# Optimization experiments

Hardware: AMD Instinct MI355X
Metric: run time of the kernel (lower is better)

Reference implementation:

```python
import jax, jax.numpy as jnp
import numpy as np

def setup_inputs() -> dict:
    key = jax.random.key(0)
    ks = jax.random.split(key, 6)
    ch, cr = 256, 32  # cr = ch // 8
    B, H, W = 4, 64, 64
    sc = 1.0 / np.sqrt(ch)
    return {
        "inputs": jax.random.normal(ks[0], (B, H, W, ch), jnp.float32),
        "Wf": jax.random.normal(ks[1], (ch, cr), jnp.float32) * sc,
        "bf": jnp.zeros((cr,), jnp.float32),
        "Wg": jax.random.normal(ks[2], (ch, cr), jnp.float32) * sc,
        "bg": jnp.zeros((cr,), jnp.float32),
        "Wh": jax.random.normal(ks[3], (ch, cr), jnp.float32) * sc,
        "bh": jnp.zeros((cr,), jnp.float32),
        "Wv": jax.random.normal(ks[4], (cr, ch), jnp.float32) * (1.0 / np.sqrt(cr)),
        "bv": jnp.zeros((ch,), jnp.float32),
        "gamma": jnp.zeros((1,), jnp.float32),
    }

def reference(inputs, Wf, bf, Wg, bg, Wh, bh, Wv, bv, gamma):
    B, H, W, C = inputs.shape
    x = inputs.reshape(B, H * W, C)  # [B, N, C]
    f = x @ Wf + bf  # [B, N, cr] (keys)
    g = x @ Wg + bg  # [B, N, cr] (queries)
    h = x @ Wh + bh  # [B, N, cr] (values)
    s = jnp.einsum('bnk,bmk->bnm', g, f)  # [B, N, N]
    beta = jax.nn.softmax(s, axis=-1)
    v = jnp.einsum('bnm,bmk->bnk', beta, h)  # [B, N, cr]
    o = v @ Wv + bv  # [B, N, C]
    out = gamma * o + x
    return out.reshape(B, H, W, C)
```

## Files before the change

kernel.cpp:

```cpp
#include <hip/hip_runtime.h>

#define B_SZ  4
#define N_TOK 4096
#define CH    256
#define CR    32
#define SEG   512
#define KT    64
#define NITER (SEG / KT)
#define LOG2E 1.44269504f

typedef __attribute__((ext_vector_type(8))) short bf16x8;
typedef __attribute__((ext_vector_type(4))) float f32x4;

__device__ inline ushort f2bf(float x) {
    uint u = __float_as_uint(x);
    u += 0x7fff + ((u >> 16) & 1);
    return (ushort)(u >> 16);
}
__device__ inline uint pk2bf(float a, float b) {
    return __builtin_amdgcn_perm(__float_as_uint(b), __float_as_uint(a), 0x07060302);
}
__device__ inline float fast_exp2(float x) {
#if __has_builtin(__builtin_amdgcn_exp2f)
    return __builtin_amdgcn_exp2f(x);
#else
    return exp2f(x);
#endif
}

__global__ __launch_bounds__(256) void proj_kernel(
    const float* __restrict__ x,
    const float* __restrict__ Wf, const float* __restrict__ Wg, const float* __restrict__ Wh,
    const float* __restrict__ bf_, const float* __restrict__ bg, const float* __restrict__ bh,
    ushort* __restrict__ fo, ushort* __restrict__ go, ushort* __restrict__ hto)
{
    __shared__ ushort wst[3][32][264];
    int t = threadIdx.x;

    {
        float4 r4[8];
        const float* rf = (const float*)&r4[0];
        #pragma unroll
        for (int q4 = 0; q4 < 8; ++q4) r4[q4] = *(const float4*)(Wf + (size_t)t * CR + q4 * 4);
        #pragma unroll
        for (int j = 0; j < 32; ++j) wst[0][j][t] = f2bf(rf[j]);
        #pragma unroll
        for (int q4 = 0; q4 < 8; ++q4) r4[q4] = *(const float4*)(Wg + (size_t)t * CR + q4 * 4);
        #pragma unroll
        for (int j = 0; j < 32; ++j) wst[1][j][t] = f2bf(rf[j]);
        #pragma unroll
        for (int q4 = 0; q4 < 8; ++q4) r4[q4] = *(const float4*)(Wh + (size_t)t * CR + q4 * 4);
        #pragma unroll
        for (int j = 0; j < 32; ++j) wst[2][j][t] = f2bf(rf[j]);
    }
    __syncthreads();

    int wv = t >> 6, L = t & 63, nl = L & 15, Q = L >> 4;
    int row_t = blockIdx.x * 64 + wv * 16;
    int b = row_t >> 12, tok0 = row_t & 4095;

    const float* xrow = x + (size_t)(row_t + nl) * CH;
    f32x4 A[6];
    #pragma unroll
    for (int i = 0; i < 6; ++i) A[i] = (f32x4){0.f, 0.f, 0.f, 0.f};

    #pragma unroll
    for (int kk = 0; kk < 8; ++kk) {
        int off = kk * 32 + Q * 8;
        float4 lo = *(const float4*)(xrow + off);
        float4 hi = *(const float4*)(xrow + off + 4);
        bf16x8 xa;
        xa[0] = (short)f2bf(lo.x); xa[1] = (short)f2bf(lo.y);
        xa[2] = (short)f2bf(lo.z); xa[3] = (short)f2bf(lo.w);
        xa[4] = (short)f2bf(hi.x); xa[5] = (short)f2bf(hi.y);
        xa[6] = (short)f2bf(hi.z); xa[7] = (short)f2bf(hi.w);

        bf16x8 wf0 = *(const bf16x8*)&wst[0][nl][off];
        bf16x8 wf1 = *(const bf16x8*)&wst[0][16 + nl][off];
        bf16x8 wg0 = *(const bf16x8*)&wst[1][nl][off];
        bf16x8 wg1 = *(const bf16x8*)&wst[1][16 + nl][off];
        bf16x8 wh0 = *(const bf16x8*)&wst[2][nl][off];
        bf16x8 wh1 = *(const bf16x8*)&wst[2][16 + nl][off];

        A[0] = __builtin_amdgcn_mfma_f32_16x16x32_bf16(xa, wf0, A[0], 0, 0, 0);
        A[1] = __builtin_amdgcn_mfma_f32_16x16x32_bf16(xa, wf1, A[1], 0, 0, 0);
        A[2] = __builtin_amdgcn_mfma_f32_16x16x32_bf16(xa, wg0, A[2], 0, 0, 0);
        A[3] = __builtin_amdgcn_mfma_f32_16x16x32_bf16(xa, wg1, A[3], 0, 0, 0);
        A[4] = __builtin_amdgcn_mfma_f32_16x16x32_bf16(wh0, xa, A[4], 0, 0, 0);
        A[5] = __builtin_amdgcn_mfma_f32_16x16x32_bf16(wh1, xa, A[5], 0, 0, 0);
    }

    float bF0 = bf_[nl], bF1 = bf_[16 + nl];
    float bG0 = bg[nl] * LOG2E, bG1 = bg[16 + nl] * LOG2E;
    #pragma unroll
    for (int r = 0; r < 4; ++r) {
        size_t ro = (size_t)(row_t + Q * 4 + r) * CR;
        fo[ro + nl]      = f2bf(A[0][r] + bF0);
        fo[ro + 16 + nl] = f2bf(A[1][r] + bF1);
        go[ro + nl]      = f2bf(fmaf(A[2][r], LOG2E, bG0));
        go[ro + 16 + nl] = f2bf(fmaf(A[3][r], LOG2E, bG1));
    }
    ushort* hb = hto + (size_t)b * CR * N_TOK + tok0 + nl;
    #pragma unroll
    for (int r = 0; r < 4; ++r) {
        int ch = Q * 4 + r;
        hb[(size_t)ch * N_TOK]        = f2bf(A[4][r] + bh[ch]);
        hb[(size_t)(16 + ch) * N_TOK] = f2bf(A[5][r] + bh[16 + ch]);
    }
}

__global__ __launch_bounds__(512, 4) void attn_kernel(
    const ushort* __restrict__ f, const ushort* __restrict__ g,
    const ushort* __restrict__ ht, const float* __restrict__ Wv,
    const float* __restrict__ bv, const float* __restrict__ gamma,
    const float* __restrict__ x, float* __restrict__ out)
{
    __shared__ unsigned long long smem_raw[38912 / 8];
    ushort (*pls)[32][76]  = (ushort (*)[32][76])smem_raw;
    float  (*obuf)[32][33] = (float (*)[32][33])smem_raw;
    float  (*lbuf)[32]     = (float (*)[32])((char*)smem_raw + 33792);
    ushort (*oc)[48]       = (ushort (*)[48])((char*)smem_raw + 34816);

    int t  = threadIdx.x;
    int wv = t >> 6;
    int L  = t & 63;
    int nl = L & 15;
    int Q  = L >> 4;
    int bid = blockIdx.x;
    int swz = (bid & 7) * 64 + (bid >> 3);
    int b  = swz >> 7;
    int q0 = (swz & 127) * 32;

    const ushort* fb  = f  + (size_t)b * N_TOK * CR;
    const ushort* htb = ht + (size_t)b * CR * N_TOK;

    bf16x8 gB0 = *(const bf16x8*)(g + ((size_t)b * N_TOK + q0 + nl) * CR + Q * 8);
    bf16x8 gB1 = *(const bf16x8*)(g + ((size_t)b * N_TOK + q0 + 16 + nl) * CR + Q * 8);

    f32x4 acc00 = {0,0,0,0}, acc01 = {0,0,0,0};
    f32x4 acc10 = {0,0,0,0}, acc11 = {0,0,0,0};
    const f32x4 zf = {0,0,0,0};
    float lsum0 = 0.f, lsum1 = 0.f;

    int key0 = wv * SEG;
    bf16x8 Ac0 = *(const bf16x8*)(fb + (size_t)(key0 +  0 + nl) * CR + Q * 8);
    bf16x8 Ac1 = *(const bf16x8*)(fb + (size_t)(key0 + 16 + nl) * CR + Q * 8);
    bf16x8 Ac2 = *(const bf16x8*)(fb + (size_t)(key0 + 32 + nl) * CR + Q * 8);
    bf16x8 Ac3 = *(const bf16x8*)(fb + (size_t)(key0 + 48 + nl) * CR + Q * 8);

    #pragma unroll 2
    for (int it = 0; it < NITER; ++it) {
        int kc = wv * SEG + it * KT;
        const ushort* hk = htb + (size_t)nl * N_TOK + kc;
        bf16x8 b00 = *(const bf16x8*)(hk + Q * 8);
        bf16x8 b01 = *(const bf16x8*)(hk + (size_t)16 * N_TOK + Q * 8);
        bf16x8 b10 = *(const bf16x8*)(hk + 32 + Q * 8);
        bf16x8 b11 = *(const bf16x8*)(hk + (size_t)16 * N_TOK + 32 + Q * 8);
        int kn = wv * SEG + ((it + 1 < NITER) ? it + 1 : 0) * KT;
        const ushort* fn = fb + (size_t)kn * CR;
        bf16x8 An0 = *(const bf16x8*)(fn + (size_t)( 0 + nl) * CR + Q * 8);
        bf16x8 An1 = *(const bf16x8*)(fn + (size_t)(16 + nl) * CR + Q * 8);
        bf16x8 An2 = *(const bf16x8*)(fn + (size_t)(32 + nl) * CR + Q * 8);
        bf16x8 An3 = *(const bf16x8*)(fn + (size_t)(48 + nl) * CR + Q * 8);

        f32x4 s00 = __builtin_amdgcn_mfma_f32_16x16x32_bf16(Ac0, gB0, zf, 0, 0, 0);
        f32x4 s01 = __builtin_amdgcn_mfma_f32_16x16x32_bf16(Ac1, gB0, zf, 0, 0, 0);
        f32x4 s02 = __builtin_amdgcn_mfma_f32_16x16x32_bf16(Ac2, gB0, zf, 0, 0, 0);
        f32x4 s03 = __builtin_amdgcn_mfma_f32_16x16x32_bf16(Ac3, gB0, zf, 0, 0, 0);
        f32x4 s10 = __builtin_amdgcn_mfma_f32_16x16x32_bf16(Ac0, gB1, zf, 0, 0, 0);
        f32x4 s11 = __builtin_amdgcn_mfma_f32_16x16x32_bf16(Ac1, gB1, zf, 0, 0, 0);
        f32x4 s12 = __builtin_amdgcn_mfma_f32_16x16x32_bf16(Ac2, gB1, zf, 0, 0, 0);
        f32x4 s13 = __builtin_amdgcn_mfma_f32_16x16x32_bf16(Ac3, gB1, zf, 0, 0, 0);

        #pragma unroll
        for (int qh = 0; qh < 2; ++qh) {
            f32x4 v0 = qh ? s10 : s00, v1 = qh ? s11 : s01;
            f32x4 v2 = qh ? s12 : s02, v3 = qh ? s13 : s03;
            int row = qh * 16 + nl;
            float p0 = fast_exp2(v0[0]), p1 = fast_exp2(v0[1]);
            float p2 = fast_exp2(v0[2]), p3 = fast_exp2(v0[3]);
            float s4 = ((p0+p1)+(p2+p3));
            uint2 w; w.x = pk2bf(p0,p1); w.y = pk2bf(p2,p3);
            *(uint2*)&pls[wv][row][ 0 + Q * 4] = w;
            p0 = fast_exp2(v1[0]); p1 = fast_exp2(v1[1]);
            p2 = fast_exp2(v1[2]); p3 = fast_exp2(v1[3]);
            s4 += ((p0+p1)+(p2+p3));
            w.x = pk2bf(p0,p1); w.y = pk2bf(p2,p3);
            *(uint2*)&pls[wv][row][16 + Q * 4] = w;
            p0 = fast_exp2(v2[0]); p1 = fast_exp2(v2[1]);
            p2 = fast_exp2(v2[2]); p3 = fast_exp2(v2[3]);
            s4 += ((p0+p1)+(p2+p3));
            w.x = pk2bf(p0,p1); w.y = pk2bf(p2,p3);
            *(uint2*)&pls[wv][row][32 + Q * 4] = w;
            p0 = fast_exp2(v3[0]); p1 = fast_exp2(v3[1]);
            p2 = fast_exp2(v3[2]); p3 = fast_exp2(v3[3]);
            s4 += ((p0+p1)+(p2+p3));
            w.x = pk2bf(p0,p1); w.y = pk2bf(p2,p3);
            *(uint2*)&pls[wv][row][48 + Q * 4] = w;
            if (qh) lsum1 += s4; else lsum0 += s4;
        }

        bf16x8 aP00 = *(const bf16x8*)&pls[wv][     nl][ 0 + Q * 8];
        bf16x8 aP01 = *(const bf16x8*)&pls[wv][     nl][32 + Q * 8];
        bf16x8 aP10 = *(const bf16x8*)&pls[wv][16 + nl][ 0 + Q * 8];
        bf16x8 aP11 = *(const bf16x8*)&pls[wv][16 + nl][32 + Q * 8];

        acc00 = __builtin_amdgcn_mfma_f32_16x16x32_bf16(aP00, b00, acc00, 0, 0, 0);
        acc01 = __builtin_amdgcn_mfma_f32_16x16x32_bf16(aP00, b01, acc01, 0, 0, 0);
        acc10 = __builtin_amdgcn_mfma_f32_16x16x32_bf16(aP10, b00, acc10, 0, 0, 0);
        acc11 = __builtin_amdgcn_mfma_f32_16x16x32_bf16(aP10, b01, acc11, 0, 0, 0);
        acc00 = __builtin_amdgcn_mfma_f32_16x16x32_bf16(aP01, b10, acc00, 0, 0, 0);
        acc01 = __builtin_amdgcn_mfma_f32_16x16x32_bf16(aP01, b11, acc01, 0, 0, 0);
        acc10 = __builtin_amdgcn_mfma_f32_16x16x32_bf16(aP11, b10, acc10, 0, 0, 0);
        acc11 = __builtin_amdgcn_mfma_f32_16x16x32_bf16(aP11, b11, acc11, 0, 0, 0);

        Ac0 = An0; Ac1 = An1; Ac2 = An2; Ac3 = An3;
    }

    lsum0 += __shfl_xor(lsum0, 16); lsum0 += __shfl_xor(lsum0, 32);
    lsum1 += __shfl_xor(lsum1, 16); lsum1 += __shfl_xor(lsum1, 32);

    __syncthreads();
    #pragma unroll
    for (int r = 0; r < 4; ++r) {
        obuf[wv][     Q * 4 + r][nl]      = acc00[r];
        obuf[wv][     Q * 4 + r][16 + nl] = acc01[r];
        obuf[wv][16 + Q * 4 + r][nl]      = acc10[r];
        obuf[wv][16 + Q * 4 + r][16 + nl] = acc11[r];
    }
    if (L < 16) { lbuf[wv][nl] = lsum0; lbuf[wv][16 + nl] = lsum1; }
    __syncthreads();

    {
        int ch = t & 31, qb = t >> 5;
        #pragma unroll
        for (int qq = qb; qq < 32; qq += 16) {
            float s = 0.f, Lq = 0.f;
            #pragma unroll
            for (int w = 0; w < 8; ++w) { s += obuf[w][qq][ch]; Lq += lbuf[w][qq]; }
            oc[qq][ch] = f2bf(s / Lq);
        }
    }
    __syncthreads();

    bf16x8 aO0 = *(const bf16x8*)&oc[     nl][Q * 8];
    bf16x8 aO1 = *(const bf16x8*)&oc[16 + nl][Q * 8];
    float gm = gamma[0];
    const float* xb = x   + ((size_t)b * N_TOK + q0) * CH;
    float*       ob = out + ((size_t)b * N_TOK + q0) * CH;
    #pragma unroll
    for (int i = 0; i < 2; ++i) {
        int nb = wv * 2 + i;
        int c = nb * 16 + nl;
        const float* wvp = Wv + c;
        bf16x8 bW;
        #pragma unroll
        for (int j = 0; j < 8; ++j) bW[j] = (short)f2bf(wvp[(size_t)(Q * 8 + j) * CH]);
        f32x4 d0 = __builtin_amdgcn_mfma_f32_16x16x32_bf16(aO0, bW, zf, 0, 0, 0);
        f32x4 d1 = __builtin_amdgcn_mfma_f32_16x16x32_bf16(aO1, bW, zf, 0, 0, 0);
        float bvc = bv[c];
        #pragma unroll
        for (int r = 0; r < 4; ++r) {
            int qa = Q * 4 + r;
            ob[qa * CH + c]        = fmaf(gm, d0[r] + bvc, xb[qa * CH + c]);
            ob[(16 + qa) * CH + c] = fmaf(gm, d1[r] + bvc, xb[(16 + qa) * CH + c]);
        }
    }
}

extern "C" void kernel_launch(void* const* d_in, const int* in_sizes, int n_in,
                              void* d_out, int out_size, void* d_ws, size_t ws_size,
                              hipStream_t stream) {
    const float* x     = (const float*)d_in[0];
    const float* Wf    = (const float*)d_in[1];
    const float* bf_   = (const float*)d_in[2];
    const float* Wg    = (const float*)d_in[3];
    const float* bg    = (const float*)d_in[4];
    const float* Wh    = (const float*)d_in[5];
    const float* bh    = (const float*)d_in[6];
    const float* Wv    = (const float*)d_in[7];
    const float* bv    = (const float*)d_in[8];
    const float* gamma = (const float*)d_in[9];
    float* out = (float*)d_out;

    const size_t T = (size_t)B_SZ * N_TOK * CR;
    ushort* fo  = (ushort*)d_ws;
    ushort* go  = fo + T;
    ushort* hto = go + T;

    proj_kernel<<<B_SZ * N_TOK / 64, 256, 0, stream>>>(x, Wf, Wg, Wh, bf_, bg, bh, fo, go, hto);
    attn_kernel<<<B_SZ * (N_TOK / 32), 512, 0, stream>>>(fo, go, hto, Wv, bv, gamma, x, out);
}
```

Before: 120.8 us.

## Use 64-query blocks of 16 waves with halved key segments per wave

Each block now handles 64 queries with 1024 threads (16 waves), each wave covering a 256-key segment in 32-key steps against all 64 queries. Every loaded K/V tile is reused across four query groups rather than two, which halves global key/value traffic per query. The cross-wave reduction now runs in two phases: the upper 8 waves write partial accumulators and the lower 8 waves add theirs into the same buffer. In exchange, shared memory rises to about 80KB per block and blocks are larger, which may lower occupancy and increase synchronisation cost.

```diff
diff --git a/kernel.cpp b/kernel.cpp
--- a/kernel.cpp
+++ b/kernel.cpp
@@ -4,8 +4,8 @@
 #define N_TOK 4096
 #define CH    256
 #define CR    32
-#define SEG   512
-#define KT    64
+#define SEG   256
+#define KT    32
 #define NITER (SEG / KT)
 #define LOG2E 1.44269504f
 
@@ -109,17 +109,17 @@
     }
 }
 
-__global__ __launch_bounds__(512, 4) void attn_kernel(
+__global__ __launch_bounds__(1024, 4) void attn_kernel(
     const ushort* __restrict__ f, const ushort* __restrict__ g,
     const ushort* __restrict__ ht, const float* __restrict__ Wv,
     const float* __restrict__ bv, const float* __restrict__ gamma,
     const float* __restrict__ x, float* __restrict__ out)
 {
-    __shared__ unsigned long long smem_raw[38912 / 8];
-    ushort (*pls)[32][76]  = (ushort (*)[32][76])smem_raw;
-    float  (*obuf)[32][33] = (float (*)[32][33])smem_raw;
-    float  (*lbuf)[32]     = (float (*)[32])((char*)smem_raw + 33792);
-    ushort (*oc)[48]       = (ushort (*)[48])((char*)smem_raw + 34816);
+    __shared__ unsigned long long smem_raw[81920 / 8];
+    ushort (*pls)[64][40]  = (ushort (*)[64][40])smem_raw;
+    float  (*obuf)[64][33] = (float (*)[64][33])smem_raw;
+    float  (*lbuf)[64]     = (float (*)[64])((char*)smem_raw + 67584);
+    ushort (*oc)[48]       = (ushort (*)[48])((char*)smem_raw + 71680);
 
     int t  = threadIdx.x;
     int wv = t >> 6;
@@ -127,143 +127,137 @@
     int nl = L & 15;
     int Q  = L >> 4;
     int bid = blockIdx.x;
-    int swz = (bid & 7) * 64 + (bid >> 3);
-    int b  = swz >> 7;
-    int q0 = (swz & 127) * 32;
+    int swz = (bid & 7) * 32 + (bid >> 3);
+    int b  = swz >> 6;
+    int q0 = (swz & 63) * 64;
 
     const ushort* fb  = f  + (size_t)b * N_TOK * CR;
     const ushort* htb = ht + (size_t)b * CR * N_TOK;
 
-    bf16x8 gB0 = *(const bf16x8*)(g + ((size_t)b * N_TOK + q0 + nl) * CR + Q * 8);
-    bf16x8 gB1 = *(const bf16x8*)(g + ((size_t)b * N_TOK + q0 + 16 + nl) * CR + Q * 8);
-
-    f32x4 acc00 = {0,0,0,0}, acc01 = {0,0,0,0};
-    f32x4 acc10 = {0,0,0,0}, acc11 = {0,0,0,0};
+    bf16x8 gB[4];
+    #pragma unroll
+    for (int qh = 0; qh < 4; ++qh)
+        gB[qh] = *(const bf16x8*)(g + ((size_t)b * N_TOK + q0 + qh * 16 + nl) * CR + Q * 8);
+
+    f32x4 acc[4][2];
+    #pragma unroll
+    for (int i = 0; i < 4; ++i) { acc[i][0] = (f32x4){0,0,0,0}; acc[i][1] = (f32x4){0,0,0,0}; }
     const f32x4 zf = {0,0,0,0};
-    float lsum0 = 0.f, lsum1 = 0.f;
+    float ls0 = 0.f, ls1 = 0.f, ls2 = 0.f, ls3 = 0.f;
 
     int key0 = wv * SEG;
-    bf16x8 Ac0 = *(const bf16x8*)(fb + (size_t)(key0 +  0 + nl) * CR + Q * 8);
+    bf16x8 Ac0 = *(const bf16x8*)(fb + (size_t)(key0 +      nl) * CR + Q * 8);
     bf16x8 Ac1 = *(const bf16x8*)(fb + (size_t)(key0 + 16 + nl) * CR + Q * 8);
-    bf16x8 Ac2 = *(const bf16x8*)(fb + (size_t)(key0 + 32 + nl) * CR + Q * 8);
-    bf16x8 Ac3 = *(const bf16x8*)(fb + (size_t)(key0 + 48 + nl) * CR + Q * 8);
 
     #pragma unroll 2
     for (int it = 0; it < NITER; ++it) {
-        int kc = wv * SEG + it * KT;
+        int kc = key0 + it * KT;
         const ushort* hk = htb + (size_t)nl * N_TOK + kc;
-        bf16x8 b00 = *(const bf16x8*)(hk + Q * 8);
-        bf16x8 b01 = *(const bf16x8*)(hk + (size_t)16 * N_TOK + Q * 8);
-        bf16x8 b10 = *(const bf16x8*)(hk + 32 + Q * 8);
-        bf16x8 b11 = *(const bf16x8*)(hk + (size_t)16 * N_TOK + 32 + Q * 8);
-        int kn = wv * SEG + ((it + 1 < NITER) ? it + 1 : 0) * KT;
-        const ushort* fn = fb + (size_t)kn * CR;
-        bf16x8 An0 = *(const bf16x8*)(fn + (size_t)( 0 + nl) * CR + Q * 8);
-        bf16x8 An1 = *(const bf16x8*)(fn + (size_t)(16 + nl) * CR + Q * 8);
-        bf16x8 An2 = *(const bf16x8*)(fn + (size_t)(32 + nl) * CR + Q * 8);
-        bf16x8 An3 = *(const bf16x8*)(fn + (size_t)(48 + nl) * CR + Q * 8);
-
-        f32x4 s00 = __builtin_amdgcn_mfma_f32_16x16x32_bf16(Ac0, gB0, zf, 0, 0, 0);
-        f32x4 s01 = __builtin_amdgcn_mfma_f32_16x16x32_bf16(Ac1, gB0, zf, 0, 0, 0);
-        f32x4 s02 = __builtin_amdgcn_mfma_f32_16x16x32_bf16(Ac2, gB0, zf, 0, 0, 0);
-        f32x4 s03 = __builtin_amdgcn_mfma_f32_16x16x32_bf16(Ac3, gB0, zf, 0, 0, 0);
-        f32x4 s10 = __builtin_amdgcn_mfma_f32_16x16x32_bf16(Ac0, gB1, zf, 0, 0, 0);
-        f32x4 s11 = __builtin_amdgcn_mfma_f32_16x16x32_bf16(Ac1, gB1, zf, 0, 0, 0);
-        f32x4 s12 = __builtin_amdgcn_mfma_f32_16x16x32_bf16(Ac2, gB1, zf, 0, 0, 0);
-        f32x4 s13 = __builtin_amdgcn_mfma_f32_16x16x32_bf16(Ac3, gB1, zf, 0, 0, 0);
-
-        #pragma unroll
-        for (int qh = 0; qh < 2; ++qh) {
-            f32x4 v0 = qh ? s10 : s00, v1 = qh ? s11 : s01;
-            f32x4 v2 = qh ? s12 : s02, v3 = qh ? s13 : s03;
+        bf16x8 bh0 = *(const bf16x8*)(hk + Q * 8);
+        bf16x8 bh1 = *(const bf16x8*)(hk + (size_t)16 * N_TOK + Q * 8);
+        int kn = key0 + ((it + 1 < NITER) ? it + 1 : 0) * KT;
+        bf16x8 An0 = *(const bf16x8*)(fb + (size_t)(kn +      nl) * CR + Q * 8);
+        bf16x8 An1 = *(const bf16x8*)(fb + (size_t)(kn + 16 + nl) * CR + Q * 8);
+
+        #pragma unroll
+        for (int qh = 0; qh < 4; ++qh) {
+            f32x4 s0 = __builtin_amdgcn_mfma_f32_16x16x32_bf16(Ac0, gB[qh], zf, 0, 0, 0);
+            f32x4 s1 = __builtin_amdgcn_mfma_f32_16x16x32_bf16(Ac1, gB[qh], zf, 0, 0, 0);
             int row = qh * 16 + nl;
-            float p0 = fast_exp2(v0[0]), p1 = fast_exp2(v0[1]);
-            float p2 = fast_exp2(v0[2]), p3 = fast_exp2(v0[3]);
-            float s4 = ((p0+p1)+(p2+p3));
-            uint2 w; w.x = pk2bf(p0,p1); w.y = pk2bf(p2,p3);
+            float p0 = fast_exp2(s0[0]), p1 = fast_exp2(s0[1]);
+            float p2 = fast_exp2(s0[2]), p3 = fast_exp2(s0[3]);
+            float s4 = ((p0 + p1) + (p2 + p3));
+            uint2 w; w.x = pk2bf(p0, p1); w.y = pk2bf(p2, p3);
             *(uint2*)&pls[wv][row][ 0 + Q * 4] = w;
-            p0 = fast_exp2(v1[0]); p1 = fast_exp2(v1[1]);
-            p2 = fast_exp2(v1[2]); p3 = fast_exp2(v1[3]);
-            s4 += ((p0+p1)+(p2+p3));
-            w.x = pk2bf(p0,p1); w.y = pk2bf(p2,p3);
+            p0 = fast_exp2(s1[0]); p1 = fast_exp2(s1[1]);
+            p2 = fast_exp2(s1[2]); p3 = fast_exp2(s1[3]);
+            s4 += ((p0 + p1) + (p2 + p3));
+            w.x = pk2bf(p0, p1); w.y = pk2bf(p2, p3);
             *(uint2*)&pls[wv][row][16 + Q * 4] = w;
-            p0 = fast_exp2(v2[0]); p1 = fast_exp2(v2[1]);
-            p2 = fast_exp2(v2[2]); p3 = fast_exp2(v2[3]);
-            s4 += ((p0+p1)+(p2+p3));
-            w.x = pk2bf(p0,p1); w.y = pk2bf(p2,p3);
-            *(uint2*)&pls[wv][row][32 + Q * 4] = w;
-            p0 = fast_exp2(v3[0]); p1 = fast_exp2(v3[1]);
-            p2 = fast_exp2(v3[2]); p3 = fast_exp2(v3[3]);
-            s4 += ((p0+p1)+(p2+p3));
-            w.x = pk2bf(p0,p1); w.y = pk2bf(p2,p3);
-            *(uint2*)&pls[wv][row][48 + Q * 4] = w;
-            if (qh) lsum1 += s4; else lsum0 += s4;
+            if (qh == 0) ls0 += s4; else if (qh == 1) ls1 += s4;
+            else if (qh == 2) ls2 += s4; else ls3 += s4;
         }
 
-        bf16x8 aP00 = *(const bf16x8*)&pls[wv][     nl][ 0 + Q * 8];
-        bf16x8 aP01 = *(const bf16x8*)&pls[wv][     nl][32 + Q * 8];
-        bf16x8 aP10 = *(const bf16x8*)&pls[wv][16 + nl][ 0 + Q * 8];
-        bf16x8 aP11 = *(const bf16x8*)&pls[wv][16 + nl][32 + Q * 8];
-
-        acc00 = __builtin_amdgcn_mfma_f32_16x16x32_bf16(aP00, b00, acc00, 0, 0, 0);
-        acc01 = __builtin_amdgcn_mfma_f32_16x16x32_bf16(aP00, b01, acc01, 0, 0, 0);
-        acc10 = __builtin_amdgcn_mfma_f32_16x16x32_bf16(aP10, b00, acc10, 0, 0, 0);
-        acc11 = __builtin_amdgcn_mfma_f32_16x16x32_bf16(aP10, b01, acc11, 0, 0, 0);
-        acc00 = __builtin_amdgcn_mfma_f32_16x16x32_bf16(aP01, b10, acc00, 0, 0, 0);
-        acc01 = __builtin_amdgcn_mfma_f32_16x16x32_bf16(aP01, b11, acc01, 0, 0, 0);
-        acc10 = __builtin_amdgcn_mfma_f32_16x16x32_bf16(aP11, b10, acc10, 0, 0, 0);
-        acc11 = __builtin_amdgcn_mfma_f32_16x16x32_bf16(aP11, b11, acc11, 0, 0, 0);
-
-        Ac0 = An0; Ac1 = An1; Ac2 = An2; Ac3 = An3;
-    }
-
-    lsum0 += __shfl_xor(lsum0, 16); lsum0 += __shfl_xor(lsum0, 32);
-    lsum1 += __shfl_xor(lsum1, 16); lsum1 += __shfl_xor(lsum1, 32);
-
-    __syncthreads();
-    #pragma unroll
-    for (int r = 0; r < 4; ++r) {
-        obuf[wv][     Q * 4 + r][nl]      = acc00[r];
-        obuf[wv][     Q * 4 + r][16 + nl] = acc01[r];
-        obuf[wv][16 + Q * 4 + r][nl]      = acc10[r];
-        obuf[wv][16 + Q * 4 + r][16 + nl] = acc11[r];
-    }
-    if (L < 16) { lbuf[wv][nl] = lsum0; lbuf[wv][16 + nl] = lsum1; }
+        bf16x8 aP0 = *(const bf16x8*)&pls[wv][     nl][Q * 8];
+        bf16x8 aP1 = *(const bf16x8*)&pls[wv][16 + nl][Q * 8];
+        bf16x8 aP2 = *(const bf16x8*)&pls[wv][32 + nl][Q * 8];
+        bf16x8 aP3 = *(const bf16x8*)&pls[wv][48 + nl][Q * 8];
+
+        acc[0][0] = __builtin_amdgcn_mfma_f32_16x16x32_bf16(aP0, bh0, acc[0][0], 0, 0, 0);
+        acc[0][1] = __builtin_amdgcn_mfma_f32_16x16x32_bf16(aP0, bh1, acc[0][1], 0, 0, 0);
+        acc[1][0] = __builtin_amdgcn_mfma_f32_16x16x32_bf16(aP1, bh0, acc[1][0], 0, 0, 0);
+        acc[1][1] = __builtin_amdgcn_mfma_f32_16x16x32_bf16(aP1, bh1, acc[1][1], 0, 0, 0);
+        acc[2][0] = __builtin_amdgcn_mfma_f32_16x16x32_bf16(aP2, bh0, acc[2][0], 0, 0, 0);
+        acc[2][1] = __builtin_amdgcn_mfma_f32_16x16x32_bf16(aP2, bh1, acc[2][1], 0, 0, 0);
+        acc[3][0] = __builtin_amdgcn_mfma_f32_16x16x32_bf16(aP3, bh0, acc[3][0], 0, 0, 0);
+        acc[3][1] = __builtin_amdgcn_mfma_f32_16x16x32_bf16(aP3, bh1, acc[3][1], 0, 0, 0);
+
+        Ac0 = An0; Ac1 = An1;
+    }
+
+    ls0 += __shfl_xor(ls0, 16); ls0 += __shfl_xor(ls0, 32);
+    ls1 += __shfl_xor(ls1, 16); ls1 += __shfl_xor(ls1, 32);
+    ls2 += __shfl_xor(ls2, 16); ls2 += __shfl_xor(ls2, 32);
+    ls3 += __shfl_xor(ls3, 16); ls3 += __shfl_xor(ls3, 32);
+
+    __syncthreads();
+
+    if (wv >= 8) {
+        #pragma unroll
+        for (int qh = 0; qh < 4; ++qh)
+            #pragma unroll
+            for (int r = 0; r < 4; ++r) {
+                obuf[wv - 8][qh * 16 + Q * 4 + r][nl]      = acc[qh][0][r];
+                obuf[wv - 8][qh * 16 + Q * 4 + r][16 + nl] = acc[qh][1][r];
+            }
+    }
+    if (L < 16) {
+        lbuf[wv][     nl] = ls0; lbuf[wv][16 + nl] = ls1;
+        lbuf[wv][32 + nl] = ls2; lbuf[wv][48 + nl] = ls3;
+    }
+    __syncthreads();
+    if (wv < 8) {
+        #pragma unroll
+        for (int qh = 0; qh < 4; ++qh)
+            #pragma unroll
+            for (int r = 0; r < 4; ++r) {
+                obuf[wv][qh * 16 + Q * 4 + r][nl]      += acc[qh][0][r];
+                obuf[wv][qh * 16 + Q * 4 + r][16 + nl] += acc[qh][1][r];
+            }
+    }
     __syncthreads();
 
     {
         int ch = t & 31, qb = t >> 5;
         #pragma unroll
-        for (int qq = qb; qq < 32; qq += 16) {
+        for (int qq = qb; qq < 64; qq += 32) {
             float s = 0.f, Lq = 0.f;
             #pragma unroll
-            for (int w = 0; w < 8; ++w) { s += obuf[w][qq][ch]; Lq += lbuf[w][qq]; }
+            for (int w = 0; w < 8; ++w) s += obuf[w][qq][ch];
+            #pragma unroll
+            for (int w = 0; w < 16; ++w) Lq += lbuf[w][qq];
             oc[qq][ch] = f2bf(s / Lq);
         }
     }
     __syncthreads();
 
-    bf16x8 aO0 = *(const bf16x8*)&oc[     nl][Q * 8];
-    bf16x8 aO1 = *(const bf16x8*)&oc[16 + nl][Q * 8];
     float gm = gamma[0];
     const float* xb = x   + ((size_t)b * N_TOK + q0) * CH;
     float*       ob = out + ((size_t)b * N_TOK + q0) * CH;
-    #pragma unroll
-    for (int i = 0; i < 2; ++i) {
-        int nb = wv * 2 + i;
-        int c = nb * 16 + nl;
-        const float* wvp = Wv + c;
-        bf16x8 bW;
-        #pragma unroll
-        for (int j = 0; j < 8; ++j) bW[j] = (short)f2bf(wvp[(size_t)(Q * 8 + j) * CH]);
-        f32x4 d0 = __builtin_amdgcn_mfma_f32_16x16x32_bf16(aO0, bW, zf, 0, 0, 0);
-        f32x4 d1 = __builtin_amdgcn_mfma_f32_16x16x32_bf16(aO1, bW, zf, 0, 0, 0);
-        float bvc = bv[c];
+    int c = wv * 16 + nl;
+    const float* wvp = Wv + c;
+    bf16x8 bW;
+    #pragma unroll
+    for (int j = 0; j < 8; ++j) bW[j] = (short)f2bf(wvp[(size_t)(Q * 8 + j) * CH]);
+    float bvc = bv[c];
+    #pragma unroll
+    for (int qg = 0; qg < 4; ++qg) {
+        bf16x8 aO = *(const bf16x8*)&oc[qg * 16 + nl][Q * 8];
+        f32x4 d = __builtin_amdgcn_mfma_f32_16x16x32_bf16(aO, bW, zf, 0, 0, 0);
         #pragma unroll
         for (int r = 0; r < 4; ++r) {
-            int qa = Q * 4 + r;
-            ob[qa * CH + c]        = fmaf(gm, d0[r] + bvc, xb[qa * CH + c]);
-            ob[(16 + qa) * CH + c] = fmaf(gm, d1[r] + bvc, xb[(16 + qa) * CH + c]);
+            int qa = qg * 16 + Q * 4 + r;
+            ob[qa * CH + c] = fmaf(gm, d[r] + bvc, xb[qa * CH + c]);
         }
     }
 }
@@ -289,5 +283,5 @@
     ushort* hto = go + T;
 
     proj_kernel<<<B_SZ * N_TOK / 64, 256, 0, stream>>>(x, Wf, Wg, Wh, bf_, bg, bh, fo, go, hto);
-    attn_kernel<<<B_SZ * (N_TOK / 32), 512, 0, stream>>>(fo, go, hto, Wv, bv, gamma, x, out);
-}
+    attn_kernel<<<B_SZ * (N_TOK / 64), 1024, 0, stream>>>(fo, go, hto, Wv, bv, gamma, x, out);
+}
```

New measurement: 112.6 us. 1.07x faster.
